# Optimization experiments

Measured on AMD Instinct MI355X. Metric: run time of the kernel, lower is better.

## Reference

```python
import jax, jax.numpy as jnp
import numpy as np

ALPHA = 0.2  # LeakyReLU negative slope (init arg alpha)


def setup_inputs() -> dict:
    key = jax.random.key(0)
    k1, k2, k3 = jax.random.split(key, 3)
    B, N, F_in, F_out = 8, 2048, 256, 256
    inp = jax.random.normal(k1, (B, N, F_in), dtype=jnp.float32)
    adj = jnp.ones((B, N, N), dtype=jnp.float32)  # unused by the module's forward
    # xavier_uniform with gain=1.414
    gain = 1.414
    bW = gain * np.sqrt(6.0 / (F_in + F_out))
    W = jax.random.uniform(k2, (F_in, F_out), minval=-bW, maxval=bW, dtype=jnp.float32)
    ba = gain * np.sqrt(6.0 / (2 * F_out + 1))
    a = jax.random.uniform(k3, (2 * F_out, 1), minval=-ba, maxval=ba, dtype=jnp.float32)
    return {"inp": inp, "adj": adj, "W": W, "a": a}


def reference(inp, adj, W, a):
    # inp: [B, N, F_in]; W: [F_in, F_out]; a: [2*F_out, 1]. adj is unused (as in source).
    F_out = W.shape[1]
    h = jnp.matmul(inp, W)  # [B, N, F_out]
    # e[b,i,j] = leakyrelu(a1 . h_i + a2 . h_j)  (equivalent to the repeat+cat+matmul)
    a1 = a[:F_out, 0]
    a2 = a[F_out:, 0]
    s1 = jnp.einsum('bnf,f->bn', h, a1)  # [B, N]
    s2 = jnp.einsum('bnf,f->bn', h, a2)  # [B, N]
    e = jax.nn.leaky_relu(s1[:, :, None] + s2[:, None, :], negative_slope=ALPHA)  # [B, N, N]
    # global per-batch min-max normalization, then affine *30 - 20
    mn = jnp.min(e, axis=(1, 2), keepdims=True)
    mx = jnp.max(e, axis=(1, 2), keepdims=True)
    e = (e - mn) / (mx - mn) * 30.0 - 20.0
    attention = jax.nn.sigmoid(e)  # dropout p=0 / eval: identity
    h_prime = jnp.matmul(attention, h)  # [B, N, F_out]
    h_prime = jax.nn.elu(h_prime)  # concat=True branch
    return h_prime, attention
```

## Files before the change

### kernel.cpp

```cpp
#include <hip/hip_runtime.h>
#include <stdint.h>

#define B_   8
#define N_   2048
#define F_   256
#define BN_  (B_ * N_)
#define ALPHA_ 0.2f

typedef __attribute__((ext_vector_type(8))) short  short8;
typedef __attribute__((ext_vector_type(4))) float  f32x4;

__device__ __forceinline__ unsigned short f2bf(float x) {
  uint32_t u = __float_as_uint(x);
  uint32_t r = (u + 0x7fffu + ((u >> 16) & 1u)) >> 16;
  return (unsigned short)r;
}

__device__ __forceinline__ uint32_t fkey(float f) {
  uint32_t b = __float_as_uint(f);
  return b ^ (uint32_t)(((int32_t)b >> 31) | (int32_t)0x80000000);
}
__device__ __forceinline__ float ikey(uint32_t k) {
  uint32_t b = (k & 0x80000000u) ? (k ^ 0x80000000u) : ~k;
  return __uint_as_float(b);
}

__device__ __forceinline__ void async_load16(const void* g, void* l) {
  __builtin_amdgcn_global_load_lds(
      (const __attribute__((address_space(1))) uint32_t*)g,
      (__attribute__((address_space(3))) uint32_t*)l, 16, 0, 0);
}

__device__ __forceinline__ void nt_store4(float* p, f32x4 v) {
  __builtin_nontemporal_store(v, (f32x4*)p);
}

__global__ void k_cvt_w(const float* __restrict__ W, unsigned short* __restrict__ WT) {
  int k = blockIdx.x, n = threadIdx.x;
  WT[n * F_ + k] = f2bf(W[k * F_ + n]);
}

__launch_bounds__(256, 1)
__global__ void k_gemm1(const float* __restrict__ inp,
                        const unsigned short* __restrict__ WT,
                        const float* __restrict__ avec,
                        unsigned short* __restrict__ hT,
                        float* __restrict__ s1g, float* __restrict__ s2g,
                        uint32_t* __restrict__ maxk, uint32_t* __restrict__ mink) {
  __shared__ __align__(16) unsigned short Atile[64 * 32];
  __shared__ __align__(16) unsigned short Btile[256 * 32];
  __shared__ __align__(16) unsigned short Trans[256 * 72];
  __shared__ float s1_lds[64], s2_lds[64];

  const int tid  = threadIdx.x;
  const int wave = tid >> 6, lane = tid & 63;
  const int n16  = lane & 15, quad = lane >> 4;
  const int i0   = blockIdx.x * 64;
  const int b    = i0 >> 11;

  if (tid < 64) { s1_lds[tid] = 0.0f; s2_lds[tid] = 0.0f; }

  f32x4 acc[4][4];
  #pragma unroll
  for (int mt = 0; mt < 4; ++mt)
    #pragma unroll
    for (int nt = 0; nt < 4; ++nt) acc[mt][nt] = (f32x4){0.f, 0.f, 0.f, 0.f};

  for (int k0 = 0; k0 < F_; k0 += 32) {
    {
      int r = tid >> 2, cp = tid & 3;
      const float* gp = inp + (size_t)(i0 + r) * F_ + k0 + cp * 8;
      float4 va = *(const float4*)gp;
      float4 vb = *(const float4*)(gp + 4);
      short8 sv;
      sv[0] = (short)f2bf(va.x); sv[1] = (short)f2bf(va.y);
      sv[2] = (short)f2bf(va.z); sv[3] = (short)f2bf(va.w);
      sv[4] = (short)f2bf(vb.x); sv[5] = (short)f2bf(vb.y);
      sv[6] = (short)f2bf(vb.z); sv[7] = (short)f2bf(vb.w);
      *(short8*)((char*)Atile + r * 64 + cp * 16) = sv;
    }
    #pragma unroll
    for (int g4 = 0; g4 < 4; ++g4) {
      int f = (wave << 6) + (g4 << 4) + (lane >> 2);
      int p = lane & 3;
      async_load16(WT + (size_t)f * F_ + k0 + p * 8,
                   (char*)Btile + wave * 4096 + g4 * 1024);
    }
    __syncthreads();

    short8 af[4], bf_[4];
    #pragma unroll
    for (int mt = 0; mt < 4; ++mt)
      af[mt] = *(const short8*)((const char*)Atile + ((mt * 16 + n16) * 64 + quad * 16));
    #pragma unroll
    for (int nt = 0; nt < 4; ++nt)
      bf_[nt] = *(const short8*)((const char*)Btile + ((wave * 64 + nt * 16 + n16) * 64 + quad * 16));
    #pragma unroll
    for (int mt = 0; mt < 4; ++mt)
      #pragma unroll
      for (int nt = 0; nt < 4; ++nt)
        acc[mt][nt] = __builtin_amdgcn_mfma_f32_16x16x32_bf16(af[mt], bf_[nt], acc[mt][nt], 0, 0, 0);
    __syncthreads();
  }

  #pragma unroll
  for (int mt = 0; mt < 4; ++mt)
    #pragma unroll
    for (int nt = 0; nt < 4; ++nt) {
      int f = (wave << 6) + (nt << 4) + n16;
      int i = (mt << 4) + (quad << 2);
      ushort4 pk;
      pk.x = f2bf(acc[mt][nt][0]); pk.y = f2bf(acc[mt][nt][1]);
      pk.z = f2bf(acc[mt][nt][2]); pk.w = f2bf(acc[mt][nt][3]);
      *(ushort4*)(Trans + f * 72 + i) = pk;
    }

  float a1v[4], a2v[4];
  #pragma unroll
  for (int nt = 0; nt < 4; ++nt) {
    int f = (wave << 6) + (nt << 4) + n16;
    a1v[nt] = avec[f];
    a2v[nt] = avec[F_ + f];
  }
  #pragma unroll
  for (int mt = 0; mt < 4; ++mt) {
    float s1p[4] = {0, 0, 0, 0}, s2p[4] = {0, 0, 0, 0};
    #pragma unroll
    for (int nt = 0; nt < 4; ++nt)
      #pragma unroll
      for (int rg = 0; rg < 4; ++rg) {
        s1p[rg] = fmaf(acc[mt][nt][rg], a1v[nt], s1p[rg]);
        s2p[rg] = fmaf(acc[mt][nt][rg], a2v[nt], s2p[rg]);
      }
    #pragma unroll
    for (int rg = 0; rg < 4; ++rg) {
      float v1 = s1p[rg], v2 = s2p[rg];
      #pragma unroll
      for (int off = 1; off < 16; off <<= 1) {
        v1 += __shfl_xor(v1, off);
        v2 += __shfl_xor(v2, off);
      }
      if (n16 == 0) {
        atomicAdd(&s1_lds[(mt << 4) + (quad << 2) + rg], v1);
        atomicAdd(&s2_lds[(mt << 4) + (quad << 2) + rg], v2);
      }
    }
  }
  __syncthreads();

  #pragma unroll
  for (int it = 0; it < 8; ++it) {
    int f = it * 32 + wave * 8 + (lane >> 3);
    int i = (lane & 7) * 8;
    short8 v = *(const short8*)(Trans + f * 72 + i);
    *(short8*)(hT + (size_t)f * BN_ + i0 + i) = v;
  }

  if (tid < 64) {
    float v1 = s1_lds[tid], v2 = s2_lds[tid];
    s1g[i0 + tid] = v1;
    s2g[i0 + tid] = v2;
    float mn1 = v1, mx1 = v1, mn2 = v2, mx2 = v2;
    #pragma unroll
    for (int off = 1; off < 64; off <<= 1) {
      mn1 = fminf(mn1, __shfl_xor(mn1, off));
      mx1 = fmaxf(mx1, __shfl_xor(mx1, off));
      mn2 = fminf(mn2, __shfl_xor(mn2, off));
      mx2 = fmaxf(mx2, __shfl_xor(mx2, off));
    }
    if (tid == 0) {
      atomicMax(&maxk[b * 2 + 0], fkey(mx1));
      atomicMax(&maxk[b * 2 + 1], fkey(mx2));
      atomicMin(&mink[b * 2 + 0], fkey(mn1));
      atomicMin(&mink[b * 2 + 1], fkey(mn2));
    }
  }
}

__launch_bounds__(256, 2)
__global__ void k_gemm2(const unsigned short* __restrict__ hT,
                        const float* __restrict__ s1, const float* __restrict__ s2,
                        const uint32_t* __restrict__ maxk, const uint32_t* __restrict__ mink,
                        float* __restrict__ hprime,
                        float* __restrict__ att) {
  __shared__ __align__(16) unsigned short Atile[32 * 32];
  __shared__ __align__(16) unsigned short Btile[256 * 32];

  const int tid  = threadIdx.x;
  const int wave = tid >> 6, lane = tid & 63;
  const int n16  = lane & 15, quad = lane >> 4;
  const int blk  = blockIdx.x;
  const int b    = blk & 7;
  const int i0   = (blk >> 3) * 32;

  float mx1 = ikey(maxk[b * 2 + 0]), mx2 = ikey(maxk[b * 2 + 1]);
  float mn1 = ikey(mink[b * 2 + 0]), mn2 = ikey(mink[b * 2 + 1]);
  float smn = mn1 + mn2, smx = mx1 + mx2;
  float emn = fmaxf(smn, ALPHA_ * smn);
  float emx = fmaxf(smx, ALPHA_ * smx);
  float scale  = 30.0f / (emx - emn);
  const float uscale = -scale;
  const float ubias  = emn * scale + 20.0f;

  const int r_att = tid >> 3;
  const int c_att = tid & 7;
  const float s1v = s1[b * N_ + i0 + r_att];
  const float* s2b = s2 + b * N_;
  float* attrow = att + ((size_t)(b * N_ + i0 + r_att)) * N_;

  f32x4 acc[2][4];
  #pragma unroll
  for (int mt = 0; mt < 2; ++mt)
    #pragma unroll
    for (int nt = 0; nt < 4; ++nt) acc[mt][nt] = (f32x4){0.f, 0.f, 0.f, 0.f};

  for (int k0 = 0; k0 < N_; k0 += 32) {
    #pragma unroll
    for (int g4 = 0; g4 < 4; ++g4) {
      int f = (wave << 6) + (g4 << 4) + (lane >> 2);
      int p = lane & 3;
      async_load16(hT + (size_t)f * BN_ + b * N_ + k0 + p * 8,
                   (char*)Btile + wave * 4096 + g4 * 1024);
    }

    float4 va = *(const float4*)(s2b + k0 + c_att * 4);
    float v[4] = {va.x, va.y, va.z, va.w};
    ushort4 spk;
    #pragma unroll
    for (int jj = 0; jj < 4; ++jj) {
      float s = s1v + v[jj];
      float l = fmaxf(s, ALPHA_ * s);
      float u = fmaf(l, uscale, ubias);
      float p_ = __builtin_amdgcn_rcpf(1.0f + __expf(u));
      v[jj] = p_;
    }
    spk.x = f2bf(v[0]); spk.y = f2bf(v[1]); spk.z = f2bf(v[2]); spk.w = f2bf(v[3]);
    nt_store4(attrow + k0 + c_att * 4, (f32x4){v[0], v[1], v[2], v[3]});
    *(ushort4*)(Atile + tid * 4) = spk;
    __syncthreads();

    short8 af[2], bf_[4];
    #pragma unroll
    for (int mt = 0; mt < 2; ++mt)
      af[mt] = *(const short8*)((const char*)Atile + ((mt * 16 + n16) * 64 + quad * 16));
    #pragma unroll
    for (int nt = 0; nt < 4; ++nt)
      bf_[nt] = *(const short8*)((const char*)Btile + ((wave * 64 + nt * 16 + n16) * 64 + quad * 16));
    #pragma unroll
    for (int mt = 0; mt < 2; ++mt)
      #pragma unroll
      for (int nt = 0; nt < 4; ++nt)
        acc[mt][nt] = __builtin_amdgcn_mfma_f32_16x16x32_bf16(af[mt], bf_[nt], acc[mt][nt], 0, 0, 0);
    __syncthreads();
  }

  float* hp = hprime + ((size_t)(b * N_ + i0)) * F_;
  #pragma unroll
  for (int mt = 0; mt < 2; ++mt)
    #pragma unroll
    for (int nt = 0; nt < 4; ++nt) {
      int fcol = (wave << 6) + (nt << 4) + n16;
      int irow = (mt << 4) + (quad << 2);
      #pragma unroll
      for (int rg = 0; rg < 4; ++rg) {
        float x = acc[mt][nt][rg];
        float y = x > 0.0f ? x : (__expf(x) - 1.0f);
        __builtin_nontemporal_store(y, hp + (size_t)(irow + rg) * F_ + fcol);
      }
    }
}

extern "C" void kernel_launch(void* const* d_in, const int* in_sizes, int n_in,
                              void* d_out, int out_size, void* d_ws, size_t ws_size,
                              hipStream_t stream) {
  const float* inp  = (const float*)d_in[0];
  const float* W    = (const float*)d_in[2];
  const float* avec = (const float*)d_in[3];

  float* hprime = (float*)d_out;
  float* att    = (float*)d_out + (size_t)B_ * N_ * F_;

  char* ws = (char*)d_ws;
  unsigned short* WT = (unsigned short*)ws;
  unsigned short* hT = (unsigned short*)(ws + 131072);
  float* s1          = (float*)(ws + 131072 + 8388608);
  float* s2          = s1 + BN_;
  uint32_t* maxk     = (uint32_t*)(s2 + BN_);
  uint32_t* mink     = maxk + 16;

  (void)hipMemsetAsync(maxk, 0x00, 64, stream);
  (void)hipMemsetAsync(mink, 0xFF, 64, stream);

  k_cvt_w<<<F_, F_, 0, stream>>>(W, WT);
  k_gemm1<<<BN_ / 64, 256, 0, stream>>>(inp, WT, avec, hT, s1, s2, maxk, mink);
  k_gemm2<<<512, 256, 0, stream>>>(hT, s1, s2, maxk, mink, hprime, att);
}
```

Measured before the change: 282.8 us.

## Load MFMA operands directly from global and double-buffer the attention tile

Both GEMM kernels now load MFMA B-operand fragments straight from global memory into registers instead of staging them through LDS with async loads. gemm1 also drops to a 32-row tile with more blocks and two blocks per CU. gemm2 double-buffers the small attention A tile with an XOR-swizzled layout, so each k-step needs only one barrier instead of two. The aim is to cut LDS traffic and barrier stalls, at the cost of uncoalesced per-lane global reads that rely on caches to absorb the redundancy.

```diff
diff --git a/kernel.cpp b/kernel.cpp
--- a/kernel.cpp
+++ b/kernel.cpp
@@ -25,14 +25,17 @@
   return __uint_as_float(b);
 }
 
-__device__ __forceinline__ void async_load16(const void* g, void* l) {
-  __builtin_amdgcn_global_load_lds(
-      (const __attribute__((address_space(1))) uint32_t*)g,
-      (__attribute__((address_space(3))) uint32_t*)l, 16, 0, 0);
-}
-
 __device__ __forceinline__ void nt_store4(float* p, f32x4 v) {
   __builtin_nontemporal_store(v, (f32x4*)p);
+}
+
+__device__ __forceinline__ short8 pack8(float4 a, float4 b) {
+  short8 s;
+  s[0] = (short)f2bf(a.x); s[1] = (short)f2bf(a.y);
+  s[2] = (short)f2bf(a.z); s[3] = (short)f2bf(a.w);
+  s[4] = (short)f2bf(b.x); s[5] = (short)f2bf(b.y);
+  s[6] = (short)f2bf(b.z); s[7] = (short)f2bf(b.w);
+  return s;
 }
 
 __global__ void k_cvt_w(const float* __restrict__ W, unsigned short* __restrict__ WT) {
@@ -40,71 +43,56 @@
   WT[n * F_ + k] = f2bf(W[k * F_ + n]);
 }
 
-__launch_bounds__(256, 1)
+__launch_bounds__(256, 2)
 __global__ void k_gemm1(const float* __restrict__ inp,
                         const unsigned short* __restrict__ WT,
                         const float* __restrict__ avec,
                         unsigned short* __restrict__ hT,
                         float* __restrict__ s1g, float* __restrict__ s2g,
                         uint32_t* __restrict__ maxk, uint32_t* __restrict__ mink) {
-  __shared__ __align__(16) unsigned short Atile[64 * 32];
-  __shared__ __align__(16) unsigned short Btile[256 * 32];
-  __shared__ __align__(16) unsigned short Trans[256 * 72];
-  __shared__ float s1_lds[64], s2_lds[64];
+  __shared__ __align__(16) unsigned short Trans[256 * 48];
+  __shared__ float s1_lds[32], s2_lds[32];
 
   const int tid  = threadIdx.x;
   const int wave = tid >> 6, lane = tid & 63;
   const int n16  = lane & 15, quad = lane >> 4;
-  const int i0   = blockIdx.x * 64;
+  const int i0   = blockIdx.x * 32;
   const int b    = i0 >> 11;
 
-  if (tid < 64) { s1_lds[tid] = 0.0f; s2_lds[tid] = 0.0f; }
-
-  f32x4 acc[4][4];
-  #pragma unroll
-  for (int mt = 0; mt < 4; ++mt)
+  if (tid < 32) { s1_lds[tid] = 0.0f; s2_lds[tid] = 0.0f; }
+  __syncthreads();
+
+  f32x4 acc[2][4];
+  #pragma unroll
+  for (int mt = 0; mt < 2; ++mt)
     #pragma unroll
     for (int nt = 0; nt < 4; ++nt) acc[mt][nt] = (f32x4){0.f, 0.f, 0.f, 0.f};
 
+  const float* ap0 = inp + (size_t)(i0 + n16) * F_ + quad * 8;
+  const float* ap1 = ap0 + (size_t)16 * F_;
+  const unsigned short* bp = WT + (size_t)(wave * 64 + n16) * F_ + quad * 8;
+
+  #pragma unroll 2
   for (int k0 = 0; k0 < F_; k0 += 32) {
-    {
-      int r = tid >> 2, cp = tid & 3;
-      const float* gp = inp + (size_t)(i0 + r) * F_ + k0 + cp * 8;
-      float4 va = *(const float4*)gp;
-      float4 vb = *(const float4*)(gp + 4);
-      short8 sv;
-      sv[0] = (short)f2bf(va.x); sv[1] = (short)f2bf(va.y);
-      sv[2] = (short)f2bf(va.z); sv[3] = (short)f2bf(va.w);
-      sv[4] = (short)f2bf(vb.x); sv[5] = (short)f2bf(vb.y);
-      sv[6] = (short)f2bf(vb.z); sv[7] = (short)f2bf(vb.w);
-      *(short8*)((char*)Atile + r * 64 + cp * 16) = sv;
-    }
-    #pragma unroll
-    for (int g4 = 0; g4 < 4; ++g4) {
-      int f = (wave << 6) + (g4 << 4) + (lane >> 2);
-      int p = lane & 3;
-      async_load16(WT + (size_t)f * F_ + k0 + p * 8,
-                   (char*)Btile + wave * 4096 + g4 * 1024);
-    }
-    __syncthreads();
-
-    short8 af[4], bf_[4];
-    #pragma unroll
-    for (int mt = 0; mt < 4; ++mt)
-      af[mt] = *(const short8*)((const char*)Atile + ((mt * 16 + n16) * 64 + quad * 16));
+    float4 a00 = *(const float4*)(ap0 + k0);
+    float4 a01 = *(const float4*)(ap0 + k0 + 4);
+    float4 a10 = *(const float4*)(ap1 + k0);
+    float4 a11 = *(const float4*)(ap1 + k0 + 4);
+    short8 bf_[4];
     #pragma unroll
     for (int nt = 0; nt < 4; ++nt)
-      bf_[nt] = *(const short8*)((const char*)Btile + ((wave * 64 + nt * 16 + n16) * 64 + quad * 16));
-    #pragma unroll
-    for (int mt = 0; mt < 4; ++mt)
-      #pragma unroll
-      for (int nt = 0; nt < 4; ++nt)
-        acc[mt][nt] = __builtin_amdgcn_mfma_f32_16x16x32_bf16(af[mt], bf_[nt], acc[mt][nt], 0, 0, 0);
-    __syncthreads();
-  }
-
-  #pragma unroll
-  for (int mt = 0; mt < 4; ++mt)
+      bf_[nt] = *(const short8*)(bp + (size_t)nt * 16 * F_ + k0);
+    short8 af0 = pack8(a00, a01);
+    short8 af1 = pack8(a10, a11);
+    #pragma unroll
+    for (int nt = 0; nt < 4; ++nt) {
+      acc[0][nt] = __builtin_amdgcn_mfma_f32_16x16x32_bf16(af0, bf_[nt], acc[0][nt], 0, 0, 0);
+      acc[1][nt] = __builtin_amdgcn_mfma_f32_16x16x32_bf16(af1, bf_[nt], acc[1][nt], 0, 0, 0);
+    }
+  }
+
+  #pragma unroll
+  for (int mt = 0; mt < 2; ++mt)
     #pragma unroll
     for (int nt = 0; nt < 4; ++nt) {
       int f = (wave << 6) + (nt << 4) + n16;
@@ -112,7 +100,7 @@
       ushort4 pk;
       pk.x = f2bf(acc[mt][nt][0]); pk.y = f2bf(acc[mt][nt][1]);
       pk.z = f2bf(acc[mt][nt][2]); pk.w = f2bf(acc[mt][nt][3]);
-      *(ushort4*)(Trans + f * 72 + i) = pk;
+      *(ushort4*)(Trans + f * 48 + i) = pk;
     }
 
   float a1v[4], a2v[4];
@@ -123,7 +111,7 @@
     a2v[nt] = avec[F_ + f];
   }
   #pragma unroll
-  for (int mt = 0; mt < 4; ++mt) {
+  for (int mt = 0; mt < 2; ++mt) {
     float s1p[4] = {0, 0, 0, 0}, s2p[4] = {0, 0, 0, 0};
     #pragma unroll
     for (int nt = 0; nt < 4; ++nt)
@@ -149,20 +137,20 @@
   __syncthreads();
 
   #pragma unroll
-  for (int it = 0; it < 8; ++it) {
-    int f = it * 32 + wave * 8 + (lane >> 3);
-    int i = (lane & 7) * 8;
-    short8 v = *(const short8*)(Trans + f * 72 + i);
+  for (int pass = 0; pass < 4; ++pass) {
+    int f = pass * 64 + wave * 16 + (lane >> 2);
+    int i = (lane & 3) * 8;
+    short8 v = *(const short8*)(Trans + f * 48 + i);
     *(short8*)(hT + (size_t)f * BN_ + i0 + i) = v;
   }
 
-  if (tid < 64) {
+  if (tid < 32) {
     float v1 = s1_lds[tid], v2 = s2_lds[tid];
     s1g[i0 + tid] = v1;
     s2g[i0 + tid] = v2;
     float mn1 = v1, mx1 = v1, mn2 = v2, mx2 = v2;
     #pragma unroll
-    for (int off = 1; off < 64; off <<= 1) {
+    for (int off = 1; off < 32; off <<= 1) {
       mn1 = fminf(mn1, __shfl_xor(mn1, off));
       mx1 = fmaxf(mx1, __shfl_xor(mx1, off));
       mn2 = fminf(mn2, __shfl_xor(mn2, off));
@@ -183,8 +171,7 @@
                         const uint32_t* __restrict__ maxk, const uint32_t* __restrict__ mink,
                         float* __restrict__ hprime,
                         float* __restrict__ att) {
-  __shared__ __align__(16) unsigned short Atile[32 * 32];
-  __shared__ __align__(16) unsigned short Btile[256 * 32];
+  __shared__ __align__(16) unsigned short Atile[2][1024];
 
   const int tid  = threadIdx.x;
   const int wave = tid >> 6, lane = tid & 63;
@@ -208,24 +195,28 @@
   const float* s2b = s2 + b * N_;
   float* attrow = att + ((size_t)(b * N_ + i0 + r_att)) * N_;
 
+  const int wbyte  = r_att * 64 + ((c_att * 8) ^ ((r_att & 3) << 4));
+  const int rbyte0 = n16 * 64 + ((quad * 16) ^ ((n16 & 3) << 4));
+  const int rbyte1 = rbyte0 + 16 * 64;
+
+  const unsigned short* bp = hT + (size_t)(wave * 64 + n16) * BN_ + (size_t)b * N_ + quad * 8;
+
   f32x4 acc[2][4];
   #pragma unroll
   for (int mt = 0; mt < 2; ++mt)
     #pragma unroll
     for (int nt = 0; nt < 4; ++nt) acc[mt][nt] = (f32x4){0.f, 0.f, 0.f, 0.f};
 
-  for (int k0 = 0; k0 < N_; k0 += 32) {
-    #pragma unroll
-    for (int g4 = 0; g4 < 4; ++g4) {
-      int f = (wave << 6) + (g4 << 4) + (lane >> 2);
-      int p = lane & 3;
-      async_load16(hT + (size_t)f * BN_ + b * N_ + k0 + p * 8,
-                   (char*)Btile + wave * 4096 + g4 * 1024);
-    }
+  int buf = 0;
+  for (int k0 = 0; k0 < N_; k0 += 32, buf ^= 1) {
+    short8 bf_[4];
+    bf_[0] = *(const short8*)(bp + k0);
+    bf_[1] = *(const short8*)(bp + (size_t)16 * BN_ + k0);
+    bf_[2] = *(const short8*)(bp + (size_t)32 * BN_ + k0);
+    bf_[3] = *(const short8*)(bp + (size_t)48 * BN_ + k0);
 
     float4 va = *(const float4*)(s2b + k0 + c_att * 4);
     float v[4] = {va.x, va.y, va.z, va.w};
-    ushort4 spk;
     #pragma unroll
     for (int jj = 0; jj < 4; ++jj) {
       float s = s1v + v[jj];
@@ -234,24 +225,23 @@
       float p_ = __builtin_amdgcn_rcpf(1.0f + __expf(u));
       v[jj] = p_;
     }
+    nt_store4(attrow + k0 + c_att * 4, (f32x4){v[0], v[1], v[2], v[3]});
+    ushort4 spk;
     spk.x = f2bf(v[0]); spk.y = f2bf(v[1]); spk.z = f2bf(v[2]); spk.w = f2bf(v[3]);
-    nt_store4(attrow + k0 + c_att * 4, (f32x4){v[0], v[1], v[2], v[3]});
-    *(ushort4*)(Atile + tid * 4) = spk;
-    __syncthreads();
-
-    short8 af[2], bf_[4];
-    #pragma unroll
-    for (int mt = 0; mt < 2; ++mt)
-      af[mt] = *(const short8*)((const char*)Atile + ((mt * 16 + n16) * 64 + quad * 16));
-    #pragma unroll
-    for (int nt = 0; nt < 4; ++nt)
-      bf_[nt] = *(const short8*)((const char*)Btile + ((wave * 64 + nt * 16 + n16) * 64 + quad * 16));
-    #pragma unroll
-    for (int mt = 0; mt < 2; ++mt)
-      #pragma unroll
-      for (int nt = 0; nt < 4; ++nt)
-        acc[mt][nt] = __builtin_amdgcn_mfma_f32_16x16x32_bf16(af[mt], bf_[nt], acc[mt][nt], 0, 0, 0);
-    __syncthreads();
+    *(ushort4*)((char*)Atile + buf * 2048 + wbyte) = spk;
+
+    asm volatile("s_waitcnt lgkmcnt(0)" ::: "memory");
+    __builtin_amdgcn_s_barrier();
+    asm volatile("" ::: "memory");
+
+    short8 af0 = *(const short8*)((const char*)Atile + buf * 2048 + rbyte0);
+    short8 af1 = *(const short8*)((const char*)Atile + buf * 2048 + rbyte1);
+
+    #pragma unroll
+    for (int nt = 0; nt < 4; ++nt) {
+      acc[0][nt] = __builtin_amdgcn_mfma_f32_16x16x32_bf16(af0, bf_[nt], acc[0][nt], 0, 0, 0);
+      acc[1][nt] = __builtin_amdgcn_mfma_f32_16x16x32_bf16(af1, bf_[nt], acc[1][nt], 0, 0, 0);
+    }
   }
 
   float* hp = hprime + ((size_t)(b * N_ + i0)) * F_;
@@ -292,6 +282,6 @@
   (void)hipMemsetAsync(mink, 0xFF, 64, stream);
 
   k_cvt_w<<<F_, F_, 0, stream>>>(W, WT);
-  k_gemm1<<<BN_ / 64, 256, 0, stream>>>(inp, WT, avec, hT, s1, s2, maxk, mink);
+  k_gemm1<<<BN_ / 32, 256, 0, stream>>>(inp, WT, avec, hT, s1, s2, maxk, mink);
   k_gemm2<<<512, 256, 0, stream>>>(hT, s1, s2, maxk, mink, hprime, att);
 }
```

Result: slower. 311.3 us (+10.1%).

## Double-buffer hT tiles and preload s2 row into LDS in gemm2

Applied to the files above, without the earlier changes.

The attention-times-h kernel now double-buffers the B tile and the attention A tile in LDS, prefetching the next hT tile asynchronously while MFMAs run on the current one, with one barrier per iteration instead of two. The full s2 row for the batch is staged into LDS once up front instead of being read from global memory every iteration. The aim is to hide global load latency behind compute. In exchange, LDS use per block rises to roughly 44 KB, which may reduce occupancy, and correctness depends on the hand-written vmcnt waits.

```diff
diff --git a/kernel.cpp b/kernel.cpp
--- a/kernel.cpp
+++ b/kernel.cpp
@@ -183,8 +183,9 @@
                         const uint32_t* __restrict__ maxk, const uint32_t* __restrict__ mink,
                         float* __restrict__ hprime,
                         float* __restrict__ att) {
-  __shared__ __align__(16) unsigned short Atile[32 * 32];
-  __shared__ __align__(16) unsigned short Btile[256 * 32];
+  __shared__ __align__(16) unsigned short Btile[2][256 * 32];
+  __shared__ __align__(16) unsigned short Atile[2][1024];
+  __shared__ __align__(16) float s2_lds[N_];
 
   const int tid  = threadIdx.x;
   const int wave = tid >> 6, lane = tid & 63;
@@ -208,24 +209,37 @@
   const float* s2b = s2 + b * N_;
   float* attrow = att + ((size_t)(b * N_ + i0 + r_att)) * N_;
 
-  f32x4 acc[2][4];
-  #pragma unroll
-  for (int mt = 0; mt < 2; ++mt)
-    #pragma unroll
-    for (int nt = 0; nt < 4; ++nt) acc[mt][nt] = (f32x4){0.f, 0.f, 0.f, 0.f};
-
-  for (int k0 = 0; k0 < N_; k0 += 32) {
+  auto stage_b = [&](int buf_, int k0_) {
     #pragma unroll
     for (int g4 = 0; g4 < 4; ++g4) {
       int f = (wave << 6) + (g4 << 4) + (lane >> 2);
       int p = lane & 3;
-      async_load16(hT + (size_t)f * BN_ + b * N_ + k0 + p * 8,
-                   (char*)Btile + wave * 4096 + g4 * 1024);
-    }
-
-    float4 va = *(const float4*)(s2b + k0 + c_att * 4);
+      async_load16(hT + (size_t)f * BN_ + b * N_ + k0_ + p * 8,
+                   (char*)Btile + buf_ * 16384 + wave * 4096 + g4 * 1024);
+    }
+  };
+
+  #pragma unroll
+  for (int it = 0; it < 2; ++it)
+    async_load16(s2b + wave * 512 + it * 256 + lane * 4,
+                 (char*)s2_lds + wave * 2048 + it * 1024);
+  stage_b(0, 0);
+  asm volatile("s_waitcnt vmcnt(0) lgkmcnt(0)" ::: "memory");
+  __builtin_amdgcn_s_barrier();
+  asm volatile("" ::: "memory");
+
+  f32x4 acc[2][4];
+  #pragma unroll
+  for (int mt = 0; mt < 2; ++mt)
+    #pragma unroll
+    for (int nt = 0; nt < 4; ++nt) acc[mt][nt] = (f32x4){0.f, 0.f, 0.f, 0.f};
+
+  for (int t = 0; t < 64; ++t) {
+    const int cur = t & 1;
+    const int k0  = t << 5;
+
+    float4 va = *(const float4*)((const char*)s2_lds + k0 * 4 + c_att * 16);
     float v[4] = {va.x, va.y, va.z, va.w};
-    ushort4 spk;
     #pragma unroll
     for (int jj = 0; jj < 4; ++jj) {
       float s = s1v + v[jj];
@@ -234,24 +248,30 @@
       float p_ = __builtin_amdgcn_rcpf(1.0f + __expf(u));
       v[jj] = p_;
     }
+    nt_store4(attrow + k0 + c_att * 4, (f32x4){v[0], v[1], v[2], v[3]});
+    ushort4 spk;
     spk.x = f2bf(v[0]); spk.y = f2bf(v[1]); spk.z = f2bf(v[2]); spk.w = f2bf(v[3]);
-    nt_store4(attrow + k0 + c_att * 4, (f32x4){v[0], v[1], v[2], v[3]});
-    *(ushort4*)(Atile + tid * 4) = spk;
-    __syncthreads();
-
-    short8 af[2], bf_[4];
-    #pragma unroll
-    for (int mt = 0; mt < 2; ++mt)
-      af[mt] = *(const short8*)((const char*)Atile + ((mt * 16 + n16) * 64 + quad * 16));
+    *(ushort4*)((char*)Atile + cur * 2048 + tid * 8) = spk;
+
+    asm volatile("s_waitcnt vmcnt(1) lgkmcnt(0)" ::: "memory");
+    __builtin_amdgcn_s_barrier();
+    asm volatile("" ::: "memory");
+
+    short8 af0 = *(const short8*)((const char*)Atile + cur * 2048 + n16 * 64 + quad * 16);
+    short8 af1 = *(const short8*)((const char*)Atile + cur * 2048 + (16 + n16) * 64 + quad * 16);
+    short8 bf_[4];
     #pragma unroll
     for (int nt = 0; nt < 4; ++nt)
-      bf_[nt] = *(const short8*)((const char*)Btile + ((wave * 64 + nt * 16 + n16) * 64 + quad * 16));
-    #pragma unroll
-    for (int mt = 0; mt < 2; ++mt)
-      #pragma unroll
-      for (int nt = 0; nt < 4; ++nt)
-        acc[mt][nt] = __builtin_amdgcn_mfma_f32_16x16x32_bf16(af[mt], bf_[nt], acc[mt][nt], 0, 0, 0);
-    __syncthreads();
+      bf_[nt] = *(const short8*)((const char*)Btile + cur * 16384 +
+                                 (wave * 64 + nt * 16 + n16) * 64 + quad * 16);
+
+    if (t < 63) stage_b(cur ^ 1, k0 + 32);
+
+    #pragma unroll
+    for (int nt = 0; nt < 4; ++nt) {
+      acc[0][nt] = __builtin_amdgcn_mfma_f32_16x16x32_bf16(af0, bf_[nt], acc[0][nt], 0, 0, 0);
+      acc[1][nt] = __builtin_amdgcn_mfma_f32_16x16x32_bf16(af1, bf_[nt], acc[1][nt], 0, 0, 0);
+    }
   }
 
   float* hp = hprime + ((size_t)(b * N_ + i0)) * F_;
```

Measured after the change: 269.1 us. -4.8%, faster.
